# Optimization experiments

Hardware: AMD Instinct MI355X
Metric: run time of the kernel (lower is better)

## Reference

```python
import jax, jax.numpy as jnp
import numpy as np

N_NODES = 50000
N_EDGES = 800000
N_REL = 3
N_GRAPHS = 500
EMB = 128
IN_DIM = EMB * 3
HID = 256
N_CLASS = 10
N_SHAPE, N_COLOR, MAX_POS = 8, 8, 128


def rgcn_layer(h, src, dst, etype, W, root, b):
    """PyG RGCNConv with default aggr='mean':
    out[v] = sum_r mean_{(j->v) in E_r} h[j] @ W[r] + h[v] @ root + b
    Aggregate raw features per (dst, relation) bucket, then apply relation matmuls.
    """
    N, R = h.shape[0], W.shape[0]
    seg = dst * R + etype  # combined (node, relation) segment id
    sums = jax.ops.segment_sum(h[src], seg, num_segments=N * R)          # (N*R, d)
    cnt = jax.ops.segment_sum(jnp.ones(seg.shape, h.dtype), seg, num_segments=N * R)
    mean = (sums / jnp.maximum(cnt, 1.0)[:, None]).reshape(N, R, -1)     # (N, R, d)
    return jnp.einsum('nrd,rdh->nh', mean, W) + h @ root + b


def setup_inputs() -> dict:
    key = jax.random.key(0)
    ks = jax.random.split(key, 20)
    f32 = jnp.float32
    inp = {
        's': jax.random.randint(ks[0], (N_NODES,), 0, N_SHAPE),
        'c': jax.random.randint(ks[1], (N_NODES,), 0, N_COLOR),
        'p': jax.random.randint(ks[2], (N_NODES,), 0, MAX_POS),
        'edge_index': jax.random.randint(ks[3], (2, N_EDGES), 0, N_NODES),
        'edge_type': jax.random.randint(ks[4], (N_EDGES,), 0, N_REL),
        'batch': jnp.sort(jax.random.randint(ks[5], (N_NODES,), 0, N_GRAPHS)),
        'shape_emb': jax.random.normal(ks[6], (N_SHAPE, EMB), f32),
        'color_emb': jax.random.normal(ks[7], (N_COLOR, EMB), f32),
        'pos_emb': jax.random.normal(ks[8], (MAX_POS, EMB), f32),
        'W1': jax.random.normal(ks[9], (N_REL, IN_DIM, HID), f32) / np.sqrt(IN_DIM),
        'root1': jax.random.normal(ks[10], (IN_DIM, HID), f32) / np.sqrt(IN_DIM),
        'b1': jnp.zeros((HID,), f32),
        'W2': jax.random.normal(ks[11], (N_REL, HID, HID), f32) / np.sqrt(HID),
        'root2': jax.random.normal(ks[12], (HID, HID), f32) / np.sqrt(HID),
        'b2': jnp.zeros((HID,), f32),
        'lin_w': jax.random.normal(ks[13], (HID, N_CLASS), f32) / np.sqrt(HID),
        'lin_b': jnp.zeros((N_CLASS,), f32),
    }
    return inp


def reference(s, c, p, edge_index, edge_type, batch,
              shape_emb, color_emb, pos_emb,
              W1, root1, b1, W2, root2, b2, lin_w, lin_b):
    src, dst = edge_index[0], edge_index[1]
    h = jnp.concatenate([shape_emb[s], color_emb[c], pos_emb[p]], axis=-1)  # (N, 3*emb)
    h = jax.nn.relu(rgcn_layer(h, src, dst, edge_type, W1, root1, b1))
    h = jax.nn.relu(rgcn_layer(h, src, dst, edge_type, W2, root2, b2))
    # global_mean_pool over graphs
    gsum = jax.ops.segment_sum(h, batch, num_segments=N_GRAPHS)
    gcnt = jax.ops.segment_sum(jnp.ones((h.shape[0],), h.dtype), batch, num_segments=N_GRAPHS)
    pooled = gsum / jnp.maximum(gcnt, 1.0)[:, None]
    return pooled @ lin_w + lin_b
```

## Files before the change

### kernel.cpp

```cpp
#include <hip/hip_runtime.h>
#include <hip/hip_bf16.h>

#define NN 50000
#define NE 800000
#define NR 3
#define NG 500
#define NB (NN * NR)
#define NCLS 10
#define NCMB 8192
#define CHUNK 2048
#define NBLK ((NB + CHUNK - 1) / CHUNK)

#define P1_COMBO   196
#define P1_ZCNT    586
#define P1_ZPOOL   502
#define P1_TAB     576
#define P1_WF      1024
#define P1_TOTAL   (P1_COMBO + P1_ZCNT + P1_ZPOOL + P1_TAB + P1_WF)
#define P2_CNT     3125
#define P2_TB      768
#define P2_TOTAL   (P2_CNT + P2_TB)

#define L1_DPB     64
#define L1_HS      776
#define L1_BLOCKS  ((NN + L1_DPB - 1) / L1_DPB)

typedef __hip_bfloat16 bf16;
typedef __attribute__((ext_vector_type(8))) short short8;
typedef __attribute__((ext_vector_type(4))) short shortx4;
typedef __attribute__((ext_vector_type(4))) float floatx4;

static __device__ __forceinline__ float b2f(bf16 x) { return __bfloat162float(x); }
static __device__ __forceinline__ bf16  f2b(float x) { return __float2bfloat16(x); }
static __device__ __forceinline__ float bs2f(short x) {
    return __bfloat162float(*reinterpret_cast<const bf16*>(&x));
}
static __device__ __forceinline__ short f2bs(float x) {
    bf16 b = __float2bfloat16(x);
    return *reinterpret_cast<const short*>(&b);
}
static __device__ __forceinline__ int rfl(int x) {
    return __builtin_amdgcn_readfirstlane(x);
}

__global__ __launch_bounds__(256) void prep1(const int* __restrict__ s,
                                             const int* __restrict__ c,
                                             const int* __restrict__ p,
                                             const float* __restrict__ se,
                                             const float* __restrict__ ce,
                                             const float* __restrict__ pe,
                                             const float* __restrict__ W1,
                                             const float* __restrict__ root1,
                                             const float* __restrict__ W2,
                                             const float* __restrict__ root2,
                                             int* __restrict__ combo,
                                             unsigned* __restrict__ cnt,
                                             unsigned* __restrict__ poolz,
                                             float* __restrict__ tab,
                                             bf16* __restrict__ Wf) {
    int b = blockIdx.x, t = threadIdx.x;
    if (b < P1_COMBO) {
        int n = b * 256 + t;
        if (n < NN) combo[n] = (s[n] << 10) | (c[n] << 7) | p[n];
        return;
    }
    b -= P1_COMBO;
    if (b < P1_ZCNT) {
        int i = b * 256 + t;
        if (i < NB) cnt[i] = 0u;
        return;
    }
    b -= P1_ZCNT;
    if (b < P1_ZPOOL) {
        int i = b * 256 + t;
        if (i < NG * 256 + NG) poolz[i] = 0u;
        return;
    }
    b -= P1_ZPOOL;
    if (b < P1_TAB) {
        int r = b / 144, row = b % 144;
        const float* A; int segk;
        if (row < 8)       { A = se + row * 128;        segk = 0; }
        else if (row < 16) { A = ce + (row - 8) * 128;  segk = 128; }
        else               { A = pe + (row - 16) * 128; segk = 256; }
        const float* W = (r < 3) ? (W1 + (size_t)r * 384 * 256) : root1;
        float acc = 0.f;
        for (int k = 0; k < 128; ++k)
            acc += A[k] * W[(size_t)(segk + k) * 256 + t];
        tab[((size_t)r * 144 + row) * 256 + t] = acc;
        return;
    }
    b -= P1_TAB;
    {
        int idx = b * 256 + t;
        int j     = idx & 7;
        int lane  = (idx >> 3) & 63;
        int ni    = (idx >> 9) & 3;
        int chunk = (idx >> 11) & 31;
        int colblk = idx >> 16;
        int col = colblk * 64 + ni * 16 + (lane & 15);
        int k   = chunk * 32 + (lane >> 4) * 8 + j;
        float v = (k < 768) ? W2[((size_t)(k >> 8) * 256 + (k & 255)) * 256 + col]
                            : root2[(size_t)(k - 768) * 256 + col];
        Wf[idx] = f2b(v);
    }
}

__global__ __launch_bounds__(256) void prep2(const int* __restrict__ ei,
                                             const int* __restrict__ et,
                                             int* __restrict__ cnt,
                                             const float* __restrict__ tab,
                                             const float* __restrict__ b1,
                                             bf16* __restrict__ tb2) {
    int b = blockIdx.x, t = threadIdx.x;
    if (b < P2_CNT) {
        int e = b * 256 + t;
        if (e < NE) atomicAdd(&cnt[ei[NE + e] * NR + et[e]], 1);
        return;
    }
    b -= P2_CNT;
    if (b < 256) {
        int r = b >> 6, sc = b & 63, si = sc >> 3, ci = sc & 7;
        float v = tab[((size_t)r * 144 + si) * 256 + t]
                + tab[((size_t)r * 144 + 8 + ci) * 256 + t];
        if (r == 3) v += b1[t];
        tb2[(size_t)b * 256 + t] = f2b(v);
    } else {
        int bb = b - 256;
        int r = bb >> 7, pi = bb & 127;
        tb2[(size_t)(256 + bb) * 256 + t] =
            f2b(tab[((size_t)r * 144 + 16 + pi) * 256 + t]);
    }
}

__global__ __launch_bounds__(256) void prep3(const bf16* __restrict__ tb2,
                                             bf16* __restrict__ tbf) {
    int idx = blockIdx.x * 256 + threadIdx.x;
    int j = idx & 7, lane = (idx >> 3) & 63, ni = (idx >> 9) & 3;
    int rest = idx >> 11;
    int chunk = rest % 24, colblk = rest / 24;
    int col = colblk * 64 + ni * 16 + (lane & 15);
    int k   = chunk * 32 + (lane >> 4) * 8 + j;
    tbf[idx] = tb2[(size_t)k * 256 + col];
}

__global__ __launch_bounds__(256) void scan_block_sums(const int* __restrict__ cnt,
                                                       int* __restrict__ bsum) {
    __shared__ int sm[256];
    int b = blockIdx.x, t = threadIdx.x;
    int base = b * CHUNK + t * 8, s = 0;
#pragma unroll
    for (int j = 0; j < 8; ++j) { int i = base + j; if (i < NB) s += cnt[i]; }
    sm[t] = s; __syncthreads();
    for (int st = 128; st; st >>= 1) { if (t < st) sm[t] += sm[t + st]; __syncthreads(); }
    if (!t) bsum[b] = sm[0];
}

__global__ __launch_bounds__(256) void scan_write(const int* __restrict__ cnt,
                                                  const int* __restrict__ bsum,
                                                  int* __restrict__ off,
                                                  int* __restrict__ cursor) {
    int b = blockIdx.x, t = threadIdx.x;
    int bbase = 0;
    for (int i = 0; i < b; ++i) bbase += bsum[i];
    if (b == 0 && t == 0) {
        int tot = 0;
        for (int i = 0; i < NBLK; ++i) tot += bsum[i];
        off[NB] = tot;
    }
    int base = b * CHUNK + t * 8;
    int v[8], ts = 0;
#pragma unroll
    for (int j = 0; j < 8; ++j) { int i = base + j; v[j] = (i < NB) ? cnt[i] : 0; ts += v[j]; }
    int lane = t & 63, wv = t >> 6;
    int incl = ts;
    for (int d = 1; d < 64; d <<= 1) {
        int o = __shfl_up(incl, d, 64);
        if (lane >= d) incl += o;
    }
    __shared__ int wsum[4];
    if (lane == 63) wsum[wv] = incl;
    __syncthreads();
    int wbase = 0;
    for (int w = 0; w < wv; ++w) wbase += wsum[w];
    int run = bbase + wbase + incl - ts;
#pragma unroll
    for (int j = 0; j < 8; ++j) {
        int i = base + j;
        if (i < NB) { off[i] = run; cursor[i] = run; }
        run += v[j];
    }
}

__global__ __launch_bounds__(256) void scatter_edges(const int* __restrict__ ei,
                                                     const int* __restrict__ et,
                                                     const int* __restrict__ combo,
                                                     int* __restrict__ cursor,
                                                     unsigned* __restrict__ esc) {
    int e = blockIdx.x * 256 + threadIdx.x;
    if (e >= NE) return;
    int b = ei[NE + e] * NR + et[e];
    int pos = atomicAdd(&cursor[b], 1);
    int s = ei[e];
    esc[pos] = ((unsigned)s << 13) | (unsigned)combo[s];
}

__global__ __launch_bounds__(256) void l1_hist(const int* __restrict__ off,
                                               const unsigned* __restrict__ esc,
                                               const int* __restrict__ combo,
                                               const bf16* __restrict__ tbf,
                                               bf16* __restrict__ h1) {
    __shared__ __align__(16) unsigned char HIST[L1_DPB * L1_HS];
    __shared__ int SOFF[193];
    __shared__ float INV[L1_DPB][4];
    const int t = threadIdx.x;
    const int dst0 = blockIdx.x * L1_DPB;

    for (int i = t; i < (L1_DPB * L1_HS) / 4; i += 256)
        ((unsigned*)HIST)[i] = 0u;
    for (int i = t; i < 193; i += 256)
        SOFF[i] = off[min(dst0 * NR + i, NB)];
    __syncthreads();

    if (t < L1_DPB) {
        int base = 3 * t;
#pragma unroll
        for (int r = 0; r < 3; ++r) {
            int c = SOFF[base + r + 1] - SOFF[base + r];
            INV[t][r] = (c > 0) ? 1.f / (float)c : 0.f;
        }
        INV[t][3] = 1.f;
        if (dst0 + t < NN) {
            int c = combo[dst0 + t];
            HIST[t * L1_HS + 192 + (c >> 7)] = 1;
            HIST[t * L1_HS + 640 + (c & 127)] = 1;
        }
    }
    int E0 = SOFF[0], E1 = SOFF[192];
    for (int e = E0 + t; e < E1; e += 256) {
        unsigned ev = esc[e];
        int lo = 0, hi = 191;
#pragma unroll 1
        while (lo < hi) {
            int mid = (lo + hi + 1) >> 1;
            if (SOFF[mid] <= e) lo = mid; else hi = mid - 1;
        }
        int dr = lo / 3, rel = lo - dr * 3;
        int sc = (int)((ev & 8191u) >> 7), p = (int)(ev & 127u);
        int a1 = dr * L1_HS + rel * 64 + sc;
        int a2 = dr * L1_HS + 256 + rel * 128 + p;
        atomicAdd((unsigned*)&HIST[a1 & ~3], 1u << (8 * (a1 & 3)));
        atomicAdd((unsigned*)&HIST[a2 & ~3], 1u << (8 * (a2 & 3)));
    }
    __syncthreads();

    const int wave = t >> 6, lane = t & 63;
    const int quad = lane >> 4, l16 = lane & 15;
    const short8* bb = (const short8*)tbf + (size_t)wave * 24 * 4 * 64 + lane;
    floatx4 acc[4][4] = {};
#pragma unroll 4
    for (int ch = 0; ch < 24; ++ch) {
        short8 bf_[4];
        const short8* bp = bb + (size_t)ch * 4 * 64;
#pragma unroll
        for (int ni = 0; ni < 4; ++ni) bf_[ni] = bp[ni * 64];
        int kb = ch * 32 + quad * 8;
        int iv = (kb < 256) ? (kb >> 6) : ((kb - 256) >> 7);
#pragma unroll
        for (int mi = 0; mi < 4; ++mi) {
            int row = mi * 16 + l16;
            unsigned hx = *(const unsigned*)&HIST[row * L1_HS + kb];
            unsigned hy = *(const unsigned*)&HIST[row * L1_HS + kb + 4];
            float w = INV[row][iv];
            short8 af;
            af[0] = f2bs((float)(hx & 0xffu) * w);
            af[1] = f2bs((float)((hx >> 8) & 0xffu) * w);
            af[2] = f2bs((float)((hx >> 16) & 0xffu) * w);
            af[3] = f2bs((float)(hx >> 24) * w);
            af[4] = f2bs((float)(hy & 0xffu) * w);
            af[5] = f2bs((float)((hy >> 8) & 0xffu) * w);
            af[6] = f2bs((float)((hy >> 16) & 0xffu) * w);
            af[7] = f2bs((float)(hy >> 24) * w);
#pragma unroll
            for (int ni = 0; ni < 4; ++ni)
                acc[mi][ni] = __builtin_amdgcn_mfma_f32_16x16x32_bf16(af, bf_[ni], acc[mi][ni], 0, 0, 0);
        }
    }

    __syncthreads();
    short* st = (short*)HIST;
#pragma unroll
    for (int mi = 0; mi < 4; ++mi)
#pragma unroll
        for (int ni = 0; ni < 4; ++ni)
#pragma unroll
            for (int ii = 0; ii < 4; ++ii) {
                int row = mi * 16 + quad * 4 + ii;
                int col = wave * 64 + ni * 16 + l16;
                st[row * 264 + col] = f2bs(fmaxf(acc[mi][ni][ii], 0.f));
            }
    __syncthreads();
    int row = t >> 2, cb = (t & 3) * 64;
    if (dst0 + row < NN) {
#pragma unroll
        for (int j = 0; j < 8; ++j)
            *(short8*)(h1 + (size_t)(dst0 + row) * 256 + cb + j * 8) =
                *(const short8*)&st[row * 264 + cb + j * 8];
    }
}

__global__ __launch_bounds__(256, 4) void agg_all(const int* __restrict__ off,
                                                  const unsigned* __restrict__ esc,
                                                  const bf16* __restrict__ h1,
                                                  bf16* __restrict__ hagg) {
    int wave = threadIdx.x >> 6, lane = threadIdx.x & 63;
    int dst = blockIdx.x * 4 + wave;
    if (dst >= NN) return;
    int l4 = lane * 4;
    int b0 = dst * NR;
    int o0 = rfl(off[b0]),     o1 = rfl(off[b0 + 1]),
        o2 = rfl(off[b0 + 2]), o3 = rfl(off[b0 + 3]);
    int nmin = min(o1 - o0, min(o2 - o1, o3 - o2));
    float s0[4] = {}, s1[4] = {}, s2[4] = {};
    int k = 0;
    for (; k + 2 <= nmin; k += 2) {
        unsigned ea0 = esc[o0 + k], ea1 = esc[o0 + k + 1];
        unsigned eb0 = esc[o1 + k], eb1 = esc[o1 + k + 1];
        unsigned ec0 = esc[o2 + k], ec1 = esc[o2 + k + 1];
        shortx4 va0 = *(const shortx4*)(h1 + (size_t)(ea0 >> 13) * 256 + l4);
        shortx4 va1 = *(const shortx4*)(h1 + (size_t)(ea1 >> 13) * 256 + l4);
        shortx4 vb0 = *(const shortx4*)(h1 + (size_t)(eb0 >> 13) * 256 + l4);
        shortx4 vb1 = *(const shortx4*)(h1 + (size_t)(eb1 >> 13) * 256 + l4);
        shortx4 vc0 = *(const shortx4*)(h1 + (size_t)(ec0 >> 13) * 256 + l4);
        shortx4 vc1 = *(const shortx4*)(h1 + (size_t)(ec1 >> 13) * 256 + l4);
#pragma unroll
        for (int i = 0; i < 4; ++i) {
            s0[i] += bs2f(va0[i]) + bs2f(va1[i]);
            s1[i] += bs2f(vb0[i]) + bs2f(vb1[i]);
            s2[i] += bs2f(vc0[i]) + bs2f(vc1[i]);
        }
    }
    for (int j = o0 + k; j < o1; j += 2) {
        bool g = j + 1 < o1;
        unsigned e0 = esc[j], e1 = esc[g ? j + 1 : j];
        shortx4 v0 = *(const shortx4*)(h1 + (size_t)(e0 >> 13) * 256 + l4);
        shortx4 v1 = *(const shortx4*)(h1 + (size_t)(e1 >> 13) * 256 + l4);
        float m = g ? 1.f : 0.f;
#pragma unroll
        for (int i = 0; i < 4; ++i) s0[i] += bs2f(v0[i]) + bs2f(v1[i]) * m;
    }
    for (int j = o1 + k; j < o2; j += 2) {
        bool g = j + 1 < o2;
        unsigned e0 = esc[j], e1 = esc[g ? j + 1 : j];
        shortx4 v0 = *(const shortx4*)(h1 + (size_t)(e0 >> 13) * 256 + l4);
        shortx4 v1 = *(const shortx4*)(h1 + (size_t)(e1 >> 13) * 256 + l4);
        float m = g ? 1.f : 0.f;
#pragma unroll
        for (int i = 0; i < 4; ++i) s1[i] += bs2f(v0[i]) + bs2f(v1[i]) * m;
    }
    for (int j = o2 + k; j < o3; j += 2) {
        bool g = j + 1 < o3;
        unsigned e0 = esc[j], e1 = esc[g ? j + 1 : j];
        shortx4 v0 = *(const shortx4*)(h1 + (size_t)(e0 >> 13) * 256 + l4);
        shortx4 v1 = *(const shortx4*)(h1 + (size_t)(e1 >> 13) * 256 + l4);
        float m = g ? 1.f : 0.f;
#pragma unroll
        for (int i = 0; i < 4; ++i) s2[i] += bs2f(v0[i]) + bs2f(v1[i]) * m;
    }
    float inv0 = (o1 > o0) ? 1.f / (float)(o1 - o0) : 0.f;
    float inv1 = (o2 > o1) ? 1.f / (float)(o2 - o1) : 0.f;
    float inv2 = (o3 > o2) ? 1.f / (float)(o3 - o2) : 0.f;
    shortx4 w0, w1, w2;
#pragma unroll
    for (int i = 0; i < 4; ++i) {
        w0[i] = f2bs(s0[i] * inv0);
        w1[i] = f2bs(s1[i] * inv1);
        w2[i] = f2bs(s2[i] * inv2);
    }
    bf16* hd = hagg + (size_t)dst * 768 + l4;
    *(shortx4*)(hd)       = w0;
    *(shortx4*)(hd + 256) = w1;
    *(shortx4*)(hd + 512) = w2;
}

__global__ __launch_bounds__(256) void gemm_cat(const bf16* __restrict__ hagg,
                                                const bf16* __restrict__ h1,
                                                const bf16* __restrict__ Wf,
                                                const float* __restrict__ bias,
                                                const int* __restrict__ batch,
                                                float* __restrict__ pool,
                                                float* __restrict__ gcnt) {
    __shared__ short st[32 * 264];
    const int t = threadIdx.x;
    const int wave = t >> 6, lane = t & 63;
    const int quad = lane >> 4, l16 = lane & 15;
    const int row0 = blockIdx.x * 32;
    const int colblk = wave;

    const int r0 = min(row0 + l16, NN - 1);
    const int r1 = min(row0 + 16 + l16, NN - 1);
    const bf16* gA0 = hagg + (size_t)r0 * 768 + quad * 8;
    const bf16* gA1 = hagg + (size_t)r1 * 768 + quad * 8;
    const bf16* gH0 = h1 + (size_t)r0 * 256 + quad * 8;
    const bf16* gH1 = h1 + (size_t)r1 * 256 + quad * 8;
    const short8* bbase = (const short8*)Wf + (size_t)colblk * 32 * 4 * 64 + lane;

    auto loadA2 = [&](int k0, short8& a0, short8& a1) {
        if (k0 < 768) { a0 = *(const short8*)(gA0 + k0); a1 = *(const short8*)(gA1 + k0); }
        else          { a0 = *(const short8*)(gH0 + k0 - 768); a1 = *(const short8*)(gH1 + k0 - 768); }
    };
    auto loadB = [&](int chunk, short8* bf4) {
        const short8* bp = bbase + (size_t)chunk * 4 * 64;
#pragma unroll
        for (int ni = 0; ni < 4; ++ni) bf4[ni] = bp[ni * 64];
    };

    floatx4 acc[2][4] = {};
    short8 aE0, aE1, bE[4];
    short8 aO0, aO1, bO[4];
    loadA2(0, aE0, aE1);  loadB(0, bE);
    loadA2(32, aO0, aO1); loadB(1, bO);

#pragma unroll
    for (int i = 0; i < 32; i += 2) {
#pragma unroll
        for (int ni = 0; ni < 4; ++ni) {
            acc[0][ni] = __builtin_amdgcn_mfma_f32_16x16x32_bf16(aE0, bE[ni], acc[0][ni], 0, 0, 0);
            acc[1][ni] = __builtin_amdgcn_mfma_f32_16x16x32_bf16(aE1, bE[ni], acc[1][ni], 0, 0, 0);
        }
        if (i + 2 < 32) { loadA2((i + 2) * 32, aE0, aE1); loadB(i + 2, bE); }
#pragma unroll
        for (int ni = 0; ni < 4; ++ni) {
            acc[0][ni] = __builtin_amdgcn_mfma_f32_16x16x32_bf16(aO0, bO[ni], acc[0][ni], 0, 0, 0);
            acc[1][ni] = __builtin_amdgcn_mfma_f32_16x16x32_bf16(aO1, bO[ni], acc[1][ni], 0, 0, 0);
        }
        if (i + 3 < 32) { loadA2((i + 3) * 32, aO0, aO1); loadB(i + 3, bO); }
    }

#pragma unroll
    for (int mi = 0; mi < 2; ++mi) {
#pragma unroll
        for (int ni = 0; ni < 4; ++ni) {
            int n = colblk * 64 + ni * 16 + l16;
            float bn = bias[n];
#pragma unroll
            for (int ii = 0; ii < 4; ++ii) {
                int lrow = mi * 16 + quad * 4 + ii;
                float v = (row0 + lrow < NN) ? fmaxf(acc[mi][ni][ii] + bn, 0.f) : 0.f;
                st[lrow * 264 + n] = f2bs(v);
            }
        }
    }
    __syncthreads();
    int nrows = NN - row0; if (nrows > 32) nrows = 32;
    int curg = batch[row0];
    float a = 0.f, cntf = 0.f;
    for (int rr = 0; rr < nrows; ++rr) {
        int g = batch[row0 + rr];
        if (g != curg) {
            atomicAdd(&pool[(size_t)curg * 256 + t], a);
            if (t == 0) atomicAdd(&gcnt[curg], cntf);
            a = 0.f; cntf = 0.f; curg = g;
        }
        a += bs2f(st[rr * 264 + t]);
        cntf += 1.f;
    }
    atomicAdd(&pool[(size_t)curg * 256 + t], a);
    if (t == 0) atomicAdd(&gcnt[curg], cntf);
}

__global__ __launch_bounds__(256) void final_head(const float* __restrict__ pool,
                                                  const float* __restrict__ gcnt,
                                                  const float* __restrict__ lin_w,
                                                  const float* __restrict__ lin_b,
                                                  float* __restrict__ out) {
    __shared__ float sm[256];
    int g = blockIdx.x, t = threadIdx.x;
    float inv = 1.0f / fmaxf(gcnt[g], 1.0f);
    sm[t] = pool[(size_t)g * 256 + t] * inv;
    __syncthreads();
    if (t < NCLS) {
        float s = lin_b[t];
        for (int d = 0; d < 256; ++d) s += sm[d] * lin_w[d * NCLS + t];
        out[g * NCLS + t] = s;
    }
}

extern "C" void kernel_launch(void* const* d_in, const int* in_sizes, int n_in,
                              void* d_out, int out_size, void* d_ws, size_t ws_size,
                              hipStream_t stream) {
    const int*   s_idx = (const int*)d_in[0];
    const int*   c_idx = (const int*)d_in[1];
    const int*   p_idx = (const int*)d_in[2];
    const int*   ei    = (const int*)d_in[3];
    const int*   et    = (const int*)d_in[4];
    const int*   batch = (const int*)d_in[5];
    const float* se    = (const float*)d_in[6];
    const float* ce    = (const float*)d_in[7];
    const float* pe    = (const float*)d_in[8];
    const float* W1    = (const float*)d_in[9];
    const float* root1 = (const float*)d_in[10];
    const float* b1    = (const float*)d_in[11];
    const float* W2    = (const float*)d_in[12];
    const float* root2 = (const float*)d_in[13];
    const float* b2    = (const float*)d_in[14];
    const float* lin_w = (const float*)d_in[15];
    const float* lin_b = (const float*)d_in[16];
    float* out = (float*)d_out;

    char* w = (char*)d_ws;
    size_t o = 0;
    auto alloc = [&](size_t bytes) -> void* {
        o = (o + 15) & ~(size_t)15;
        void* ptr = w + o;
        o += bytes;
        return ptr;
    };
    bf16*     hagg   = (bf16*)    alloc((size_t)NN * 768 * 2);
    bf16*     h1     = (bf16*)    alloc((size_t)NN * 256 * 2);
    bf16*     tb2    = (bf16*)    alloc((size_t)768 * 256 * 2);
    bf16*     tbf    = (bf16*)    alloc((size_t)768 * 256 * 2);
    int*      combo  = (int*)     alloc((size_t)NN * 4);
    unsigned* esc    = (unsigned*)alloc((size_t)NE * 4);
    int*      cnt    = (int*)     alloc((size_t)NB * 4);
    int*      off    = (int*)     alloc((size_t)(NB + 1) * 4);
    int*      cursor = (int*)     alloc((size_t)NB * 4);
    int*      bsum   = (int*)     alloc((size_t)NBLK * 4);
    float*    tab    = (float*)   alloc((size_t)4 * 144 * 256 * 4);
    bf16*     Wf     = (bf16*)    alloc((size_t)256 * 1024 * 2);
    float*    pool   = (float*)   alloc((size_t)NG * 256 * 4);
    float*    gcnt   = (float*)   alloc((size_t)NG * 4);
    (void)ws_size;

    prep1<<<P1_TOTAL, 256, 0, stream>>>(s_idx, c_idx, p_idx, se, ce, pe,
                                        W1, root1, W2, root2,
                                        combo, (unsigned*)cnt, (unsigned*)pool, tab, Wf);
    prep2<<<P2_TOTAL, 256, 0, stream>>>(ei, et, cnt, tab, b1, tb2);
    prep3<<<768, 256, 0, stream>>>(tb2, tbf);
    scan_block_sums<<<NBLK, 256, 0, stream>>>(cnt, bsum);
    scan_write<<<NBLK, 256, 0, stream>>>(cnt, bsum, off, cursor);
    scatter_edges<<<(NE + 255) / 256, 256, 0, stream>>>(ei, et, combo, cursor, esc);
    l1_hist<<<L1_BLOCKS, 256, 0, stream>>>(off, esc, combo, tbf, h1);
    agg_all<<<(NN + 3) / 4, 256, 0, stream>>>(off, esc, h1, hagg);
    gemm_cat<<<(NN + 31) / 32, 256, 0, stream>>>(hagg, h1, Wf, b2, batch, pool, gcnt);
    final_head<<<NG, 256, 0, stream>>>(pool, gcnt, lin_w, lin_b, out);
}
```

Measured before the change: 388.6 us.

## Stage A tiles through per-wave LDS with row-contiguous loads and deeper prefetch

The concatenated GEMM now loads A fragments with a row-major lane mapping: four lanes cover 32 contiguous k values of one row. Each wave writes these into its own LDS slab and reads them back in the MFMA operand layout. The register double-buffer becomes a four-deep prefetch ring of A and B chunks, meant to hide more global-load latency. This adds an LDS write/read per chunk, uses more registers, and enlarges shared memory, which the epilogue reuses after a barrier.

```diff
diff --git a/kernel.cpp b/kernel.cpp
--- a/kernel.cpp
+++ b/kernel.cpp
@@ -390,19 +390,21 @@
                                                 const int* __restrict__ batch,
                                                 float* __restrict__ pool,
                                                 float* __restrict__ gcnt) {
-    __shared__ short st[32 * 264];
+    __shared__ short lds[4][4][32 * 40];
     const int t = threadIdx.x;
     const int wave = t >> 6, lane = t & 63;
     const int quad = lane >> 4, l16 = lane & 15;
     const int row0 = blockIdx.x * 32;
     const int colblk = wave;
-
-    const int r0 = min(row0 + l16, NN - 1);
-    const int r1 = min(row0 + 16 + l16, NN - 1);
-    const bf16* gA0 = hagg + (size_t)r0 * 768 + quad * 8;
-    const bf16* gA1 = hagg + (size_t)r1 * 768 + quad * 8;
-    const bf16* gH0 = h1 + (size_t)r0 * 256 + quad * 8;
-    const bf16* gH1 = h1 + (size_t)r1 * 256 + quad * 8;
+    const int rsub = lane >> 2;
+    const int ksub = (lane & 3) * 8;
+
+    const int r0 = min(row0 + rsub, NN - 1);
+    const int r1 = min(row0 + 16 + rsub, NN - 1);
+    const bf16* gA0 = hagg + (size_t)r0 * 768 + ksub;
+    const bf16* gA1 = hagg + (size_t)r1 * 768 + ksub;
+    const bf16* gH0 = h1 + (size_t)r0 * 256 + ksub;
+    const bf16* gH1 = h1 + (size_t)r1 * 256 + ksub;
     const short8* bbase = (const short8*)Wf + (size_t)colblk * 32 * 4 * 64 + lane;
 
     auto loadA2 = [&](int k0, short8& a0, short8& a1) {
@@ -416,27 +418,30 @@
     };
 
     floatx4 acc[2][4] = {};
-    short8 aE0, aE1, bE[4];
-    short8 aO0, aO1, bO[4];
-    loadA2(0, aE0, aE1);  loadB(0, bE);
-    loadA2(32, aO0, aO1); loadB(1, bO);
-
-#pragma unroll
-    for (int i = 0; i < 32; i += 2) {
-#pragma unroll
-        for (int ni = 0; ni < 4; ++ni) {
-            acc[0][ni] = __builtin_amdgcn_mfma_f32_16x16x32_bf16(aE0, bE[ni], acc[0][ni], 0, 0, 0);
-            acc[1][ni] = __builtin_amdgcn_mfma_f32_16x16x32_bf16(aE1, bE[ni], acc[1][ni], 0, 0, 0);
-        }
-        if (i + 2 < 32) { loadA2((i + 2) * 32, aE0, aE1); loadB(i + 2, bE); }
-#pragma unroll
-        for (int ni = 0; ni < 4; ++ni) {
-            acc[0][ni] = __builtin_amdgcn_mfma_f32_16x16x32_bf16(aO0, bO[ni], acc[0][ni], 0, 0, 0);
-            acc[1][ni] = __builtin_amdgcn_mfma_f32_16x16x32_bf16(aO1, bO[ni], acc[1][ni], 0, 0, 0);
-        }
-        if (i + 3 < 32) { loadA2((i + 3) * 32, aO0, aO1); loadB(i + 3, bO); }
-    }
-
+    short8 a0_[4], a1_[4], b_[4][4];
+#pragma unroll
+    for (int q = 0; q < 4; ++q) { loadA2(q * 32, a0_[q], a1_[q]); loadB(q, b_[q]); }
+
+#pragma unroll
+    for (int i = 0; i < 32; i += 4) {
+#pragma unroll
+        for (int q = 0; q < 4; ++q) {
+            int ch = i + q;
+            *(short8*)&lds[wave][q][rsub * 40 + ksub] = a0_[q];
+            *(short8*)&lds[wave][q][(16 + rsub) * 40 + ksub] = a1_[q];
+            short8 af0 = *(const short8*)&lds[wave][q][l16 * 40 + quad * 8];
+            short8 af1 = *(const short8*)&lds[wave][q][(16 + l16) * 40 + quad * 8];
+#pragma unroll
+            for (int ni = 0; ni < 4; ++ni) {
+                acc[0][ni] = __builtin_amdgcn_mfma_f32_16x16x32_bf16(af0, b_[q][ni], acc[0][ni], 0, 0, 0);
+                acc[1][ni] = __builtin_amdgcn_mfma_f32_16x16x32_bf16(af1, b_[q][ni], acc[1][ni], 0, 0, 0);
+            }
+            if (ch + 4 < 32) { loadA2((ch + 4) * 32, a0_[q], a1_[q]); loadB(ch + 4, b_[q]); }
+        }
+    }
+
+    __syncthreads();
+    short* st = &lds[0][0][0];
 #pragma unroll
     for (int mi = 0; mi < 2; ++mi) {
 #pragma unroll
```

After: 360.7 us. 7.2% less time.
